# Kernel optimization log

Hardware: AMD Instinct MI355X
Metric: run time of the kernel (lower is better)

The kernel has to match this reference:

```python
import jax, jax.numpy as jnp
import numpy as np

EPS = 1e-5

def conv1x1(x, w):
    # x: (B,C,H,W), w: (O,C) -> (B,O,H,W)
    return jnp.einsum('bchw,oc->bohw', x, w)

def bn_relu(y, g, b, m, v):
    s = g / jnp.sqrt(v + EPS)
    return jax.nn.relu(y * s[None, :, None, None] + (b - m * s)[None, :, None, None])

def cbr(x, w, g, b, m, v):
    return bn_relu(conv1x1(x, w), g, b, m, v)

def _bn_params(key, c):
    k1, k2, k3, k4 = jax.random.split(key, 4)
    g = 1.0 + 0.1 * jax.random.normal(k1, (c,), jnp.float32)
    b = 0.1 * jax.random.normal(k2, (c,), jnp.float32)
    m = 0.05 * jax.random.normal(k3, (c,), jnp.float32)
    v = jax.random.uniform(k4, (c,), jnp.float32, 0.5, 1.5)
    return g, b, m, v

def setup_inputs() -> dict:
    key = jax.random.key(0)
    B, Cin, H, W = 8, 512, 64, 64
    Ck, Cv, Cout = 256, 256, 512
    ks = jax.random.split(key, 12)
    def w(k, o, c):
        return jax.random.normal(k, (o, c), jnp.float32) * (1.0 / np.sqrt(c))
    inp = {}
    inp['x'] = jax.random.normal(ks[0], (B, Cin, H, W), jnp.float32)
    # f_key
    inp['kW1'] = w(ks[1], Ck, Cin); inp['kG1'], inp['kB1'], inp['kM1'], inp['kV1'] = _bn_params(ks[2], Ck)
    inp['kW2'] = w(ks[3], Ck, Ck);  inp['kG2'], inp['kB2'], inp['kM2'], inp['kV2'] = _bn_params(ks[4], Ck)
    # f_query
    inp['qW1'] = w(ks[5], Ck, Cin); inp['qG1'], inp['qB1'], inp['qM1'], inp['qV1'] = _bn_params(ks[6], Ck)
    inp['qW2'] = w(ks[7], Ck, Ck);  inp['qG2'], inp['qB2'], inp['qM2'], inp['qV2'] = _bn_params(ks[8], Ck)
    # f_value
    inp['vW'] = w(ks[9], Cv, Cin)
    # W (output projection)
    inp['wW'] = w(ks[10], Cout, Cv); inp['wG'], inp['wB'], inp['wM'], inp['wV'] = _bn_params(ks[11], Cout)
    return inp

def reference(x,
              kW1, kG1, kB1, kM1, kV1, kW2, kG2, kB2, kM2, kV2,
              qW1, qG1, qB1, qM1, qV1, qW2, qG2, qB2, qM2, qV2,
              vW,
              wW, wG, wB, wM, wV):
    B, _, H, W = x.shape
    q = cbr(cbr(x, qW1, qG1, qB1, qM1, qV1), qW2, qG2, qB2, qM2, qV2)  # (B,Ck,H,W)
    k = cbr(cbr(x, kW1, kG1, kB1, kM1, kV1), kW2, kG2, kB2, kM2, kV2)  # (B,Ck,H,W)
    v = conv1x1(x, vW)                                                  # (B,Cv,H,W)
    Ck = q.shape[1]; Cv = v.shape[1]; N = H * W
    qf = q.reshape(B, Ck, N)   # query = qf^T -> (B,N,Ck)
    kf = k.reshape(B, Ck, N)
    vf = v.reshape(B, Cv, N)
    sim = jnp.einsum('bcn,bcm->bnm', qf, kf) * (Ck ** -0.5)  # (B,N,N)
    attn = jax.nn.softmax(sim, axis=-1)
    ctx = jnp.einsum('bnm,bcm->bcn', attn, vf).reshape(B, Cv, H, W)
    return cbr(ctx, wW, wG, wB, wM, wV)
```

## Files before the change

### kernel.cpp

```cpp
#include <hip/hip_runtime.h>
#include <hip/hip_bf16.h>

typedef __attribute__((ext_vector_type(8))) short bf16x8;
typedef __attribute__((ext_vector_type(4))) float f32x4;

#define MFMA16(a, b, c) __builtin_amdgcn_mfma_f32_16x16x32_bf16(a, b, c, 0, 0, 0)

static __device__ __forceinline__ unsigned short f2bf(float f) {
  union { __hip_bfloat16 h; unsigned short u; } cv;
  cv.h = __float2bfloat16(f);
  return cv.u;
}

static __device__ __forceinline__ void gload16(const void* gptr, void* lptr) {
  __builtin_amdgcn_global_load_lds(
      (const __attribute__((address_space(1))) void*)gptr,
      (__attribute__((address_space(3))) void*)lptr, 16, 0, 0);
}


__global__ void conv_w_k(const float* __restrict__ qW1, const float* __restrict__ kW1,
                         const float* __restrict__ qW2, const float* __restrict__ kW2,
                         const float* __restrict__ vW, const float* __restrict__ wW,
                         __hip_bfloat16* __restrict__ dst) {
  int i = blockIdx.x * 256 + threadIdx.x;
  const float* src; int off;
  if (i < 131072)      { src = qW1; off = i; }
  else if (i < 262144) { src = kW1; off = i - 131072; }
  else if (i < 327680) { src = qW2; off = i - 262144; }
  else if (i < 393216) { src = kW2; off = i - 327680; }
  else if (i < 524288) { src = vW;  off = i - 393216; }
  else                 { src = wW;  off = i - 524288; }
  dst[i] = __float2bfloat16(src[off]);
}

__global__ void bn_all_k(const float* __restrict__ qG1, const float* __restrict__ qB1, const float* __restrict__ qM1, const float* __restrict__ qV1,
                         const float* __restrict__ qG2, const float* __restrict__ qB2, const float* __restrict__ qM2, const float* __restrict__ qV2,
                         const float* __restrict__ kG1, const float* __restrict__ kB1, const float* __restrict__ kM1, const float* __restrict__ kV1,
                         const float* __restrict__ kG2, const float* __restrict__ kB2, const float* __restrict__ kM2, const float* __restrict__ kV2,
                         const float* __restrict__ wG, const float* __restrict__ wB, const float* __restrict__ wM, const float* __restrict__ wV,
                         float* __restrict__ base) {
  int bidx = blockIdx.x, tid = threadIdx.x;
  const float *g, *b, *m, *v; float *s, *t; int i;
  if (bidx == 0)      { g = qG1; b = qB1; m = qM1; v = qV1; s = base;        t = base + 256;  i = tid; }
  else if (bidx == 1) { g = qG2; b = qB2; m = qM2; v = qV2; s = base + 512;  t = base + 768;  i = tid; }
  else if (bidx == 2) { g = kG1; b = kB1; m = kM1; v = kV1; s = base + 1024; t = base + 1280; i = tid; }
  else if (bidx == 3) { g = kG2; b = kB2; m = kM2; v = kV2; s = base + 1536; t = base + 1792; i = tid; }
  else                { g = wG;  b = wB;  m = wM;  v = wV;  s = base + 2048; t = base + 2560; i = (bidx - 4) * 256 + tid; }
  float sv = g[i] * rsqrtf(v[i] + 1e-5f);
  s[i] = sv;
  t[i] = b[i] - m[i] * sv;
}

__global__ __launch_bounds__(256) void transpose_k(const float* __restrict__ x,
                                                   __hip_bfloat16* __restrict__ xT) {
  __shared__ float tile[64][65];
  const int n0 = blockIdx.x * 64, c0 = blockIdx.y * 64, b = blockIdx.z;
  const int tx = threadIdx.x, ty = threadIdx.y;
  const float* xp = x + ((size_t)(b * 512 + c0) * 4096) + n0;
#pragma unroll
  for (int i = 0; i < 16; ++i) {
    int c = ty + 4 * i;
    tile[c][tx] = xp[(size_t)c * 4096 + tx];
  }
  __syncthreads();
  __hip_bfloat16* op = xT + ((size_t)(b * 4096 + n0) * 512) + c0;
#pragma unroll
  for (int i = 0; i < 16; ++i) {
    int nl = ty + 4 * i;
    op[(size_t)nl * 512 + tx] = __float2bfloat16(tile[tx][nl]);
  }
}

template <int EPI>
__global__ __launch_bounds__(256) void gemm_nt_k(
    const __hip_bfloat16* __restrict__ A, long sA,
    const __hip_bfloat16* __restrict__ B, long sB,
    void* __restrict__ Cp, long sC,
    int lda, int ldb, int ldc, int K,
    const float* __restrict__ s, const float* __restrict__ t) {
  __shared__ short As[128][72];
  __shared__ short Bs[128][72];
  const int tid = threadIdx.x;
  const int w = tid >> 6, l = tid & 63, g = l >> 4, ln = l & 15;
  const int wr = w >> 1, wc = w & 1;
  const int rb = blockIdx.x * 128, cb = blockIdx.y * 128;
  const __hip_bfloat16* Ab = A + (size_t)blockIdx.z * sA;
  const __hip_bfloat16* Bb = B + (size_t)blockIdx.z * sB;

  f32x4 acc[4][4];
#pragma unroll
  for (int i = 0; i < 4; ++i)
#pragma unroll
    for (int j = 0; j < 4; ++j) acc[i][j] = (f32x4){0.f, 0.f, 0.f, 0.f};

  const int r0 = tid >> 3;
  const int c8 = (tid & 7) * 8;

  for (int k0 = 0; k0 < K; k0 += 64) {
#pragma unroll
    for (int i = 0; i < 4; ++i) {
      const int r = r0 + 32 * i;
      *(uint4*)&As[r][c8] = *(const uint4*)(Ab + (size_t)(rb + r) * lda + (k0 + c8));
      *(uint4*)&Bs[r][c8] = *(const uint4*)(Bb + (size_t)(cb + r) * ldb + (k0 + c8));
    }
    __syncthreads();
#pragma unroll
    for (int kk = 0; kk < 2; ++kk) {
      bf16x8 av[4], bv[4];
#pragma unroll
      for (int i = 0; i < 4; ++i) av[i] = *(const bf16x8*)&As[64 * wr + 16 * i + ln][32 * kk + 8 * g];
#pragma unroll
      for (int i = 0; i < 4; ++i) bv[i] = *(const bf16x8*)&Bs[64 * wc + 16 * i + ln][32 * kk + 8 * g];
#pragma unroll
      for (int mi = 0; mi < 4; ++mi)
#pragma unroll
        for (int ni = 0; ni < 4; ++ni)
          acc[mi][ni] = MFMA16(av[mi], bv[ni], acc[mi][ni]);
    }
    __syncthreads();
  }

  const int row0 = rb + 64 * wr + 4 * g;
  const int col0 = cb + 64 * wc + ln;

  if (EPI == 2) {
    float* C = (float*)Cp + (size_t)blockIdx.z * sC;
#pragma unroll
    for (int mi = 0; mi < 4; ++mi) {
#pragma unroll
      for (int r = 0; r < 4; ++r) {
        const int R = row0 + 16 * mi + r;
        const float sr = s[R], tr = t[R];
#pragma unroll
        for (int ni = 0; ni < 4; ++ni) {
          float v = fmaf(acc[mi][ni][r], sr, tr);
          C[(size_t)R * ldc + (col0 + 16 * ni)] = v > 0.f ? v : 0.f;
        }
      }
    }
  } else {
    __hip_bfloat16* C = (__hip_bfloat16*)Cp + (size_t)blockIdx.z * sC;
    float sc[4], tc[4];
    if (EPI == 1) {
#pragma unroll
      for (int ni = 0; ni < 4; ++ni) { sc[ni] = s[col0 + 16 * ni]; tc[ni] = t[col0 + 16 * ni]; }
    }
#pragma unroll
    for (int mi = 0; mi < 4; ++mi) {
#pragma unroll
      for (int ni = 0; ni < 4; ++ni) {
#pragma unroll
        for (int r = 0; r < 4; ++r) {
          float v = acc[mi][ni][r];
          if (EPI == 1) { v = fmaf(v, sc[ni], tc[ni]); v = v > 0.f ? v : 0.f; }
          C[(size_t)(row0 + 16 * mi + r) * ldc + (col0 + 16 * ni)] = __float2bfloat16(v);
        }
      }
    }
  }
}

__global__ __launch_bounds__(256, 2) void flash_k(
    const __hip_bfloat16* __restrict__ Q,
    const __hip_bfloat16* __restrict__ Kt,
    const __hip_bfloat16* __restrict__ V,
    __hip_bfloat16* __restrict__ O) {
  __shared__ short Ks[64 * 256];
  __shared__ short Vs[256 * 64];
  __shared__ short Ps[4][16 * 64];

  const int tid = threadIdx.x;
  const int w = tid >> 6, l = tid & 63, g = l >> 4, ln = l & 15;
  const int bid = blockIdx.x;
  const int batch = bid & 7;
  const int qb = (bid >> 3) << 6;
  const size_t bo = (size_t)batch * (4096 * 256);
  const float CE = 0.09016844005556021f;

  bf16x8 qf[8];
  {
    const __hip_bfloat16* qp = Q + bo + (size_t)(qb + 16 * w + ln) * 256 + 8 * g;
#pragma unroll
    for (int kk = 0; kk < 8; ++kk) qf[kk] = *(const bf16x8*)(qp + 32 * kk);
  }

  f32x4 acc[16];
#pragma unroll
  for (int ci = 0; ci < 16; ++ci) acc[ci] = (f32x4){0.f, 0.f, 0.f, 0.f};
  float m_run = -1e30f, l_run = 0.f;

  const int kRow = 16 * w + (l >> 5);
  const int kChunk = (l & 31) ^ (l >> 5);
  const int vRow = 64 * w + (l >> 3);
  const int vChunk = (l & 7) ^ ((l >> 3) & 7);

  const short* Kb = (const short*)(Kt + bo);
  const short* Vb = (const short*)(V + bo);

  auto stageK = [&](int m0) {
#pragma unroll
    for (int j = 0; j < 8; ++j) {
      const short* gp = Kb + (size_t)(m0 + kRow + 2 * j) * 256 + 8 * (kChunk ^ ((2 * j) & 7));
      gload16(gp, Ks + w * 4096 + j * 512);
    }
  };
  auto stageV = [&](int m0) {
#pragma unroll
    for (int j = 0; j < 8; ++j) {
      const short* gp = Vb + (size_t)(vRow + 8 * j) * 4096 + m0 + 8 * vChunk;
      gload16(gp, Vs + w * 4096 + j * 512);
    }
  };

  stageK(0);
  stageV(0);
  __builtin_amdgcn_sched_barrier(0);

  for (int t = 0; t < 64; ++t) {
    asm volatile("s_waitcnt vmcnt(8)" ::: "memory");
    __builtin_amdgcn_sched_barrier(0);
    __builtin_amdgcn_s_barrier();
    __builtin_amdgcn_sched_barrier(0);

    f32x4 sf[4];
#pragma unroll
    for (int mi = 0; mi < 4; ++mi) sf[mi] = (f32x4){0.f, 0.f, 0.f, 0.f};
    __builtin_amdgcn_s_setprio(1);
#pragma unroll
    for (int kk = 0; kk < 8; ++kk) {
#pragma unroll
      for (int mi = 0; mi < 4; ++mi) {
        const int idx = (((16 * mi + ln) * 256) + 32 * kk + 8 * g) ^ ((ln & 7) << 3);
        bf16x8 a = *(const bf16x8*)&Ks[idx];
        sf[mi] = MFMA16(a, qf[kk], sf[mi]);
      }
    }
    __builtin_amdgcn_s_setprio(0);

    float sv[16];
#pragma unroll
    for (int mi = 0; mi < 4; ++mi)
#pragma unroll
      for (int r = 0; r < 4; ++r) sv[4 * mi + r] = sf[mi][r];
    float mmax = sv[0];
#pragma unroll
    for (int j = 1; j < 16; ++j) mmax = fmaxf(mmax, sv[j]);
    mmax = fmaxf(mmax, __shfl_xor(mmax, 16));
    mmax = fmaxf(mmax, __shfl_xor(mmax, 32));

    if (!__all((mmax - m_run) * CE <= 8.0f)) {
      float m_new = fmaxf(m_run, mmax);
      float alpha = exp2f((m_run - m_new) * CE);
      l_run *= alpha;
#pragma unroll
      for (int r = 0; r < 4; ++r) {
        float ar = __shfl(alpha, 4 * g + r);
#pragma unroll
        for (int ci = 0; ci < 16; ++ci) acc[ci][r] *= ar;
      }
      m_run = m_new;
    }
    float p[16], psum = 0.f;
#pragma unroll
    for (int j = 0; j < 16; ++j) {
      p[j] = exp2f((sv[j] - m_run) * CE);
      psum += p[j];
    }
    psum += __shfl_xor(psum, 16);
    psum += __shfl_xor(psum, 32);
    l_run += psum;

#pragma unroll
    for (int mi = 0; mi < 4; ++mi) {
      uint2 pk;
      pk.x = (unsigned int)f2bf(p[4 * mi + 0]) | ((unsigned int)f2bf(p[4 * mi + 1]) << 16);
      pk.y = (unsigned int)f2bf(p[4 * mi + 2]) | ((unsigned int)f2bf(p[4 * mi + 3]) << 16);
      const int idx = (ln * 64 + 16 * mi + 4 * g) ^ ((ln & 7) << 3);
      *(uint2*)&Ps[w][idx] = pk;
    }

    asm volatile("s_waitcnt vmcnt(0)" ::: "memory");
    __builtin_amdgcn_sched_barrier(0);
    __builtin_amdgcn_s_barrier();
    __builtin_amdgcn_sched_barrier(0);

    if (t < 63) stageK(64 * (t + 1));
    __builtin_amdgcn_sched_barrier(0);

    __builtin_amdgcn_s_setprio(1);
#pragma unroll
    for (int kk2 = 0; kk2 < 2; ++kk2) {
      const int pidx = (ln * 64 + 32 * kk2 + 8 * g) ^ ((ln & 7) << 3);
      bf16x8 pa = *(const bf16x8*)&Ps[w][pidx];
#pragma unroll
      for (int ci = 0; ci < 16; ++ci) {
        const int vidx = ((16 * ci + ln) * 64 + 32 * kk2 + 8 * g) ^ ((ln & 7) << 3);
        bf16x8 vfr = *(const bf16x8*)&Vs[vidx];
        acc[ci] = MFMA16(pa, vfr, acc[ci]);
      }
    }
    __builtin_amdgcn_s_setprio(0);

    __builtin_amdgcn_s_barrier();
    __builtin_amdgcn_sched_barrier(0);
    if (t < 63) stageV(64 * (t + 1));
    __builtin_amdgcn_sched_barrier(0);
  }

  float linv[4];
#pragma unroll
  for (int r = 0; r < 4; ++r) linv[r] = 1.0f / __shfl(l_run, 4 * g + r);

  __hip_bfloat16* Ob = O + bo;
#pragma unroll
  for (int ci = 0; ci < 16; ++ci) {
#pragma unroll
    for (int r = 0; r < 4; ++r) {
      float val = acc[ci][r] * linv[r];
      Ob[(size_t)(qb + 16 * w + 4 * g + r) * 256 + 16 * ci + ln] = __float2bfloat16(val);
    }
  }
}


extern "C" void kernel_launch(void* const* d_in, const int* in_sizes, int n_in,
                              void* d_out, int out_size, void* d_ws, size_t ws_size,
                              hipStream_t stream) {
  const float* x   = (const float*)d_in[0];
  const float* kW1 = (const float*)d_in[1];
  const float* kG1 = (const float*)d_in[2];
  const float* kB1 = (const float*)d_in[3];
  const float* kM1 = (const float*)d_in[4];
  const float* kV1 = (const float*)d_in[5];
  const float* kW2 = (const float*)d_in[6];
  const float* kG2 = (const float*)d_in[7];
  const float* kB2 = (const float*)d_in[8];
  const float* kM2 = (const float*)d_in[9];
  const float* kV2 = (const float*)d_in[10];
  const float* qW1 = (const float*)d_in[11];
  const float* qG1 = (const float*)d_in[12];
  const float* qB1 = (const float*)d_in[13];
  const float* qM1 = (const float*)d_in[14];
  const float* qV1 = (const float*)d_in[15];
  const float* qW2 = (const float*)d_in[16];
  const float* qG2 = (const float*)d_in[17];
  const float* qB2 = (const float*)d_in[18];
  const float* qM2 = (const float*)d_in[19];
  const float* qV2 = (const float*)d_in[20];
  const float* vW  = (const float*)d_in[21];
  const float* wW  = (const float*)d_in[22];
  const float* wG  = (const float*)d_in[23];
  const float* wB  = (const float*)d_in[24];
  const float* wM  = (const float*)d_in[25];
  const float* wV  = (const float*)d_in[26];

  char* ws = (char*)d_ws;
  __hip_bfloat16* bQW1 = (__hip_bfloat16*)(ws + 0);
  __hip_bfloat16* bKW1 = (__hip_bfloat16*)(ws + 262144);
  __hip_bfloat16* bQW2 = (__hip_bfloat16*)(ws + 524288);
  __hip_bfloat16* bKW2 = (__hip_bfloat16*)(ws + 655360);
  __hip_bfloat16* bVW  = (__hip_bfloat16*)(ws + 786432);
  __hip_bfloat16* bWW  = (__hip_bfloat16*)(ws + 1048576);
  float* bnBase = (float*)(ws + 1310720);
  float* sQ1 = bnBase + 0;
  float* tQ1 = bnBase + 256;
  float* sQ2 = bnBase + 512;
  float* tQ2 = bnBase + 768;
  float* sK1 = bnBase + 1024;
  float* tK1 = bnBase + 1280;
  float* sK2 = bnBase + 1536;
  float* tK2 = bnBase + 1792;
  float* sWo = bnBase + 2048;
  float* tWo = bnBase + 2560;
  __hip_bfloat16* xT   = (__hip_bfloat16*)(ws + 2097152);
  __hip_bfloat16* bufA = (__hip_bfloat16*)(ws + 35651584);
  __hip_bfloat16* q2b  = (__hip_bfloat16*)(ws + 52428800);
  __hip_bfloat16* k2b  = (__hip_bfloat16*)(ws + 69206016);
  __hip_bfloat16* vB   = (__hip_bfloat16*)(ws + 85983232);

  conv_w_k<<<2560, 256, 0, stream>>>(qW1, kW1, qW2, kW2, vW, wW, bQW1);
  bn_all_k<<<6, 256, 0, stream>>>(qG1, qB1, qM1, qV1, qG2, qB2, qM2, qV2,
                                  kG1, kB1, kM1, kV1, kG2, kB2, kM2, kV2,
                                  wG, wB, wM, wV, bnBase);

  transpose_k<<<dim3(64, 8, 8), dim3(64, 4), 0, stream>>>(x, xT);

  gemm_nt_k<1><<<dim3(32, 2, 8), 256, 0, stream>>>(xT, 2097152L, bQW1, 0L, bufA, 1048576L,
                                                   512, 512, 256, 512, sQ1, tQ1);
  gemm_nt_k<1><<<dim3(32, 2, 8), 256, 0, stream>>>(bufA, 1048576L, bQW2, 0L, q2b, 1048576L,
                                                   256, 256, 256, 256, sQ2, tQ2);
  gemm_nt_k<1><<<dim3(32, 2, 8), 256, 0, stream>>>(xT, 2097152L, bKW1, 0L, bufA, 1048576L,
                                                   512, 512, 256, 512, sK1, tK1);
  gemm_nt_k<1><<<dim3(32, 2, 8), 256, 0, stream>>>(bufA, 1048576L, bKW2, 0L, k2b, 1048576L,
                                                   256, 256, 256, 256, sK2, tK2);
  gemm_nt_k<0><<<dim3(2, 32, 8), 256, 0, stream>>>(bVW, 0L, xT, 2097152L, vB, 1048576L,
                                                   512, 512, 4096, 512, nullptr, nullptr);
  flash_k<<<512, 256, 0, stream>>>(q2b, k2b, vB, bufA);
  gemm_nt_k<2><<<dim3(4, 32, 8), 256, 0, stream>>>(bWW, 0L, bufA, 1048576L, d_out, 2097152L,
                                                   256, 256, 4096, 256, sWo, tWo);
}
```

Before: 297.4 us.

## Restructure flash attention: double-buffer K, load V to registers, split PV by channel

The flash kernel now double-buffers K tiles in LDS and loads V straight from global memory into registers, one iteration ahead, with inline asm instead of staging through LDS. The PV product is split so each wave owns 64 output channels for all 64 queries, reading a shared P tile. Rescale factors are exchanged through LDS with per-wave flags. The loop is unrolled by two to alternate buffers. This removes the V LDS round trip and one barrier stall per iteration, and overlaps loads with compute. In exchange it adds register pressure, LDS traffic for P and alpha, and hand-tuned waitcnt counts that must match the loads in flight.

```diff
diff --git a/kernel.cpp b/kernel.cpp
--- a/kernel.cpp
+++ b/kernel.cpp
@@ -166,9 +166,11 @@
     const __hip_bfloat16* __restrict__ Kt,
     const __hip_bfloat16* __restrict__ V,
     __hip_bfloat16* __restrict__ O) {
-  __shared__ short Ks[64 * 256];
-  __shared__ short Vs[256 * 64];
-  __shared__ short Ps[4][16 * 64];
+  __shared__ short Ks[2][64 * 256];
+  __shared__ short Ps[64 * 64];
+  __shared__ float aLds[64];
+  __shared__ float lLds[64];
+  __shared__ int fLds[4];
 
   const int tid = threadIdx.x;
   const int w = tid >> 6, l = tid & 63, g = l >> 4, ln = l & 15;
@@ -178,6 +180,17 @@
   const size_t bo = (size_t)batch * (4096 * 256);
   const float CE = 0.09016844005556021f;
 
+  const int swz45 = (16 * g) ^ ((ln & 3) << 4);
+  const int s6 = ((ln >> 2) & 1) << 6;
+  const char* Ka0 = (const char*)Ks[0] + (ln * 512 + swz45 + s6);
+  const char* Ka1 = Ka0 + (((ln >> 2) & 1) ? -64 : 64);
+  const char* Kb0 = Ka0 + 32768;
+  const char* Kb1 = Ka1 + 32768;
+  const char* Pr0 = (const char*)Ps + (ln * 128 + swz45 + s6);
+  const char* Pr1 = Pr0 + (((ln >> 2) & 1) ? -64 : 64);
+  const int pwOff = (16 * w + ln) * 128 + 8 * (g & 1) + (((g >> 1) ^ (ln & 1)) << 4) +
+                    (((ln >> 1) & 1) << 5) + s6;
+
   bf16x8 qf[8];
   {
     const __hip_bfloat16* qp = Q + bo + (size_t)(qb + 16 * w + ln) * 256 + 8 * g;
@@ -185,140 +198,189 @@
     for (int kk = 0; kk < 8; ++kk) qf[kk] = *(const bf16x8*)(qp + 32 * kk);
   }
 
-  f32x4 acc[16];
-#pragma unroll
-  for (int ci = 0; ci < 16; ++ci) acc[ci] = (f32x4){0.f, 0.f, 0.f, 0.f};
+  f32x4 acc[4][4];
+#pragma unroll
+  for (int qg = 0; qg < 4; ++qg)
+#pragma unroll
+    for (int ci = 0; ci < 4; ++ci) acc[qg][ci] = (f32x4){0.f, 0.f, 0.f, 0.f};
   float m_run = -1e30f, l_run = 0.f;
 
   const int kRow = 16 * w + (l >> 5);
   const int kChunk = (l & 31) ^ (l >> 5);
-  const int vRow = 64 * w + (l >> 3);
-  const int vChunk = (l & 7) ^ ((l >> 3) & 7);
-
-  const short* Kb = (const short*)(Kt + bo);
-  const short* Vb = (const short*)(V + bo);
-
-  auto stageK = [&](int m0) {
-#pragma unroll
-    for (int j = 0; j < 8; ++j) {
-      const short* gp = Kb + (size_t)(m0 + kRow + 2 * j) * 256 + 8 * (kChunk ^ ((2 * j) & 7));
-      gload16(gp, Ks + w * 4096 + j * 512);
-    }
-  };
-  auto stageV = [&](int m0) {
-#pragma unroll
-    for (int j = 0; j < 8; ++j) {
-      const short* gp = Vb + (size_t)(vRow + 8 * j) * 4096 + m0 + 8 * vChunk;
-      gload16(gp, Vs + w * 4096 + j * 512);
-    }
-  };
-
-  stageK(0);
-  stageV(0);
+  const short* kPtr[8];
+#pragma unroll
+  for (int j = 0; j < 8; ++j)
+    kPtr[j] = (const short*)(Kt + bo) + (size_t)(kRow + 2 * j) * 256 + 8 * (kChunk ^ ((2 * j) & 7));
+  const short* vPtr[4];
+#pragma unroll
+  for (int ci = 0; ci < 4; ++ci)
+    vPtr[ci] = (const short*)(V + bo) + (size_t)(64 * w + 16 * ci + ln) * 4096 + 8 * g;
+
+  bf16x8 vfrA[8], vfrB[8];
+
+#define STAGEK(NB)                                                     \
+  do {                                                                 \
+    _Pragma("unroll") for (int j = 0; j < 8; ++j) {                    \
+      gload16(kPtr[j], (short*)Ks[NB] + w * 4096 + j * 512);           \
+      kPtr[j] += 16384;                      \
+    }                                                                  \
+  } while (0)
+
+#define ISSUEV(VARR)                                                   \
+  do {                                                                 \
+    _Pragma("unroll") for (int ci = 0; ci < 4; ++ci) {                 \
+      asm volatile("global_load_dwordx4 %0, %2, off\n\t"               \
+                   "global_load_dwordx4 %1, %2, off offset:64"         \
+                   : "=&v"(VARR[2 * ci]), "=&v"(VARR[2 * ci + 1])      \
+                   : "v"(vPtr[ci]));                                   \
+      vPtr[ci] += 64;                  \
+    }                                                                  \
+  } while (0)
+
+  STAGEK(0);
   __builtin_amdgcn_sched_barrier(0);
-
-  for (int t = 0; t < 64; ++t) {
-    asm volatile("s_waitcnt vmcnt(8)" ::: "memory");
-    __builtin_amdgcn_sched_barrier(0);
-    __builtin_amdgcn_s_barrier();
-    __builtin_amdgcn_sched_barrier(0);
-
-    f32x4 sf[4];
-#pragma unroll
-    for (int mi = 0; mi < 4; ++mi) sf[mi] = (f32x4){0.f, 0.f, 0.f, 0.f};
-    __builtin_amdgcn_s_setprio(1);
-#pragma unroll
-    for (int kk = 0; kk < 8; ++kk) {
-#pragma unroll
-      for (int mi = 0; mi < 4; ++mi) {
-        const int idx = (((16 * mi + ln) * 256) + 32 * kk + 8 * g) ^ ((ln & 7) << 3);
-        bf16x8 a = *(const bf16x8*)&Ks[idx];
-        sf[mi] = MFMA16(a, qf[kk], sf[mi]);
+  ISSUEV(vfrA);
+  __builtin_amdgcn_sched_barrier(0);
+
+#define BODY(T, K0P, K1P, VCUR, VNXT, NB)                                      \
+  do {                                                                         \
+                      \
+    asm volatile("s_waitcnt vmcnt(8)" ::: "memory");                           \
+    __builtin_amdgcn_sched_barrier(0);                                         \
+                                    \
+    f32x4 sf[4];                                                               \
+    _Pragma("unroll") for (int mi = 0; mi < 4; ++mi)                           \
+        sf[mi] = (f32x4){0.f, 0.f, 0.f, 0.f};                                  \
+    __builtin_amdgcn_s_setprio(1);                                             \
+    _Pragma("unroll") for (int kk = 0; kk < 8; ++kk) {                         \
+      const char* kp = ((kk & 1) ? K1P : K0P) + 128 * (kk >> 1);               \
+      _Pragma("unroll") for (int mi = 0; mi < 4; ++mi) {                       \
+        bf16x8 a = *(const bf16x8*)(kp + 8192 * mi);                           \
+        sf[mi] = MFMA16(a, qf[kk], sf[mi]);                                    \
+      }                                                                        \
+    }                                                                          \
+    __builtin_amdgcn_s_setprio(0);                                             \
+    __builtin_amdgcn_sched_barrier(0);                                         \
+    if ((T) < 63) {                                                            \
+      STAGEK(NB);                               \
+      __builtin_amdgcn_sched_barrier(0);                                       \
+      ISSUEV(VNXT);                           \
+      __builtin_amdgcn_sched_barrier(0);                                       \
+    }                                                                          \
+                                          \
+    float sv[16];                                                              \
+    _Pragma("unroll") for (int mi = 0; mi < 4; ++mi)                           \
+        _Pragma("unroll") for (int r = 0; r < 4; ++r)                          \
+        sv[4 * mi + r] = sf[mi][r];                                            \
+    float a0 = fmaxf(fmaxf(sv[0], sv[1]), sv[2]);                              \
+    float a1 = fmaxf(fmaxf(sv[3], sv[4]), sv[5]);                              \
+    float a2 = fmaxf(fmaxf(sv[6], sv[7]), sv[8]);                              \
+    float a3 = fmaxf(fmaxf(sv[9], sv[10]), sv[11]);                            \
+    float a4 = fmaxf(fmaxf(sv[12], sv[13]), sv[14]);                           \
+    float mmax = fmaxf(fmaxf(fmaxf(fmaxf(a0, a1), a2), fmaxf(a3, a4)), sv[15]);\
+    mmax = fmaxf(mmax, __shfl_xor(mmax, 16));                                  \
+    mmax = fmaxf(mmax, __shfl_xor(mmax, 32));                                  \
+    float alpha = 1.0f;                                                        \
+    int rs = 0;                                                                \
+    if (!__all((mmax - m_run) * CE <= 8.0f)) {                                 \
+      float m_new = fmaxf(m_run, mmax);                                        \
+      alpha = exp2f((m_run - m_new) * CE);                                     \
+      l_run *= alpha;                                                          \
+      m_run = m_new;                                                           \
+      rs = 1;                                                                  \
+    }                                                                          \
+    float p[16], psum = 0.f;                                                   \
+    _Pragma("unroll") for (int j = 0; j < 16; ++j) {                           \
+      p[j] = exp2f((sv[j] - m_run) * CE);                                      \
+      psum += p[j];                                                            \
+    }                                                                          \
+    psum += __shfl_xor(psum, 16);                                              \
+    psum += __shfl_xor(psum, 32);                                              \
+    l_run += psum;                                                             \
+    {                                                                          \
+      uint2 pk0, pk1, pk2, pk3;                                                \
+      pk0.x = (unsigned)f2bf(p[0]) | ((unsigned)f2bf(p[1]) << 16);             \
+      pk0.y = (unsigned)f2bf(p[2]) | ((unsigned)f2bf(p[3]) << 16);             \
+      pk1.x = (unsigned)f2bf(p[4]) | ((unsigned)f2bf(p[5]) << 16);             \
+      pk1.y = (unsigned)f2bf(p[6]) | ((unsigned)f2bf(p[7]) << 16);             \
+      pk2.x = (unsigned)f2bf(p[8]) | ((unsigned)f2bf(p[9]) << 16);             \
+      pk2.y = (unsigned)f2bf(p[10]) | ((unsigned)f2bf(p[11]) << 16);           \
+      pk3.x = (unsigned)f2bf(p[12]) | ((unsigned)f2bf(p[13]) << 16);           \
+      pk3.y = (unsigned)f2bf(p[14]) | ((unsigned)f2bf(p[15]) << 16);           \
+      char* Pb = (char*)Ps;                                                    \
+      *(uint2*)(Pb + (pwOff ^ 0)) = pk0;                                       \
+      *(uint2*)(Pb + (pwOff ^ 32)) = pk1;                                      \
+      *(uint2*)(Pb + (pwOff ^ 64)) = pk2;                                      \
+      *(uint2*)(Pb + (pwOff ^ 96)) = pk3;                                      \
+    }                                                                          \
+    if (g == 0) aLds[16 * w + ln] = alpha;                                     \
+    if (l == 0) fLds[w] = rs;                                                  \
+                                  \
+    asm volatile("s_waitcnt lgkmcnt(0)" ::: "memory");                         \
+    __builtin_amdgcn_sched_barrier(0);                                         \
+    __builtin_amdgcn_s_barrier();                                              \
+    asm volatile("" ::: "memory");                                             \
+    __builtin_amdgcn_sched_barrier(0);                                         \
+                              \
+    {                                                                          \
+      int4 fl = *(const int4*)fLds;                                            \
+      if (fl.x | fl.y | fl.z | fl.w) {                                         \
+        _Pragma("unroll") for (int qg = 0; qg < 4; ++qg) {                     \
+          f32x4 av = *(const f32x4*)&aLds[16 * qg + 4 * g];                    \
+          _Pragma("unroll") for (int ci = 0; ci < 4; ++ci) acc[qg][ci] *= av;  \
+        }                                                                      \
+      }                                                                        \
+    }                                                                          \
+                         \
+    if ((T) < 63) {                                                            \
+      asm volatile("s_waitcnt vmcnt(16)" ::: "memory");                        \
+    } else {                                                                   \
+      asm volatile("s_waitcnt vmcnt(0)" ::: "memory");                         \
+    }                                                                          \
+    __builtin_amdgcn_sched_barrier(0);                                         \
+                              \
+    __builtin_amdgcn_s_setprio(1);                                             \
+    _Pragma("unroll") for (int kk = 0; kk < 2; ++kk) {                         \
+      _Pragma("unroll") for (int qg = 0; qg < 4; ++qg) {                       \
+        bf16x8 pa = *(const bf16x8*)((kk ? Pr1 : Pr0) + 2048 * qg);            \
+        _Pragma("unroll") for (int ci = 0; ci < 4; ++ci)                       \
+            acc[qg][ci] = MFMA16(pa, VCUR[2 * ci + kk], acc[qg][ci]);          \
+      }                                                                        \
+    }                                                                          \
+    __builtin_amdgcn_s_setprio(0);                                             \
+    __builtin_amdgcn_sched_barrier(0);                                         \
+                   \
+    __builtin_amdgcn_s_barrier();                                              \
+    asm volatile("" ::: "memory");                                             \
+    __builtin_amdgcn_sched_barrier(0);                                         \
+  } while (0)
+
+  for (int tp = 0; tp < 32; ++tp) {
+    const int t0 = 2 * tp;
+    BODY(t0, Ka0, Ka1, vfrA, vfrB, 1);
+    BODY(t0 + 1, Kb0, Kb1, vfrB, vfrA, 0);
+  }
+#undef BODY
+#undef STAGEK
+#undef ISSUEV
+
+  if (g == 0) lLds[16 * w + ln] = l_run;
+  __syncthreads();
+
+  __hip_bfloat16* Ob = O + bo;
+#pragma unroll
+  for (int qg = 0; qg < 4; ++qg) {
+    f32x4 lv = *(const f32x4*)&lLds[16 * qg + 4 * g];
+    f32x4 li;
+#pragma unroll
+    for (int r = 0; r < 4; ++r) li[r] = 1.0f / lv[r];
+#pragma unroll
+    for (int ci = 0; ci < 4; ++ci) {
+#pragma unroll
+      for (int r = 0; r < 4; ++r) {
+        float val = acc[qg][ci][r] * li[r];
+        Ob[(size_t)(qb + 16 * qg + 4 * g + r) * 256 + 64 * w + 16 * ci + ln] = __float2bfloat16(val);
       }
-    }
-    __builtin_amdgcn_s_setprio(0);
-
-    float sv[16];
-#pragma unroll
-    for (int mi = 0; mi < 4; ++mi)
-#pragma unroll
-      for (int r = 0; r < 4; ++r) sv[4 * mi + r] = sf[mi][r];
-    float mmax = sv[0];
-#pragma unroll
-    for (int j = 1; j < 16; ++j) mmax = fmaxf(mmax, sv[j]);
-    mmax = fmaxf(mmax, __shfl_xor(mmax, 16));
-    mmax = fmaxf(mmax, __shfl_xor(mmax, 32));
-
-    if (!__all((mmax - m_run) * CE <= 8.0f)) {
-      float m_new = fmaxf(m_run, mmax);
-      float alpha = exp2f((m_run - m_new) * CE);
-      l_run *= alpha;
-#pragma unroll
-      for (int r = 0; r < 4; ++r) {
-        float ar = __shfl(alpha, 4 * g + r);
-#pragma unroll
-        for (int ci = 0; ci < 16; ++ci) acc[ci][r] *= ar;
-      }
-      m_run = m_new;
-    }
-    float p[16], psum = 0.f;
-#pragma unroll
-    for (int j = 0; j < 16; ++j) {
-      p[j] = exp2f((sv[j] - m_run) * CE);
-      psum += p[j];
-    }
-    psum += __shfl_xor(psum, 16);
-    psum += __shfl_xor(psum, 32);
-    l_run += psum;
-
-#pragma unroll
-    for (int mi = 0; mi < 4; ++mi) {
-      uint2 pk;
-      pk.x = (unsigned int)f2bf(p[4 * mi + 0]) | ((unsigned int)f2bf(p[4 * mi + 1]) << 16);
-      pk.y = (unsigned int)f2bf(p[4 * mi + 2]) | ((unsigned int)f2bf(p[4 * mi + 3]) << 16);
-      const int idx = (ln * 64 + 16 * mi + 4 * g) ^ ((ln & 7) << 3);
-      *(uint2*)&Ps[w][idx] = pk;
-    }
-
-    asm volatile("s_waitcnt vmcnt(0)" ::: "memory");
-    __builtin_amdgcn_sched_barrier(0);
-    __builtin_amdgcn_s_barrier();
-    __builtin_amdgcn_sched_barrier(0);
-
-    if (t < 63) stageK(64 * (t + 1));
-    __builtin_amdgcn_sched_barrier(0);
-
-    __builtin_amdgcn_s_setprio(1);
-#pragma unroll
-    for (int kk2 = 0; kk2 < 2; ++kk2) {
-      const int pidx = (ln * 64 + 32 * kk2 + 8 * g) ^ ((ln & 7) << 3);
-      bf16x8 pa = *(const bf16x8*)&Ps[w][pidx];
-#pragma unroll
-      for (int ci = 0; ci < 16; ++ci) {
-        const int vidx = ((16 * ci + ln) * 64 + 32 * kk2 + 8 * g) ^ ((ln & 7) << 3);
-        bf16x8 vfr = *(const bf16x8*)&Vs[vidx];
-        acc[ci] = MFMA16(pa, vfr, acc[ci]);
-      }
-    }
-    __builtin_amdgcn_s_setprio(0);
-
-    __builtin_amdgcn_s_barrier();
-    __builtin_amdgcn_sched_barrier(0);
-    if (t < 63) stageV(64 * (t + 1));
-    __builtin_amdgcn_sched_barrier(0);
-  }
-
-  float linv[4];
-#pragma unroll
-  for (int r = 0; r < 4; ++r) linv[r] = 1.0f / __shfl(l_run, 4 * g + r);
-
-  __hip_bfloat16* Ob = O + bo;
-#pragma unroll
-  for (int ci = 0; ci < 16; ++ci) {
-#pragma unroll
-    for (int r = 0; r < 4; ++r) {
-      float val = acc[ci][r] * linv[r];
-      Ob[(size_t)(qb + 16 * w + 4 * g + r) * 256 + 16 * ci + ln] = __float2bfloat16(val);
     }
   }
 }
```

Result: slower. 367.8 us (+23.6%).
